# Optimization experiments

Hardware: AMD Instinct MI355X
Metric: run time of the kernel (lower is better)

The kernel has to match this reference:

```python
import jax, jax.numpy as jnp
from jax import lax
import numpy as np

Vw, Vc, TAGS = 50000, 200, 600
WE, CE, CC, H = 128, 48, 64, 256   # word emb, char emb, char cnn out, encoder hidden
B, T, CL, LMAX = 64, 96, 16, 24    # batch, seq, chars-per-word, lemma max len
HD = H // 2                        # per-direction LSTM hidden
BOS = 3


def _conv1d_same(x, w, b):
    # x: [N, Cin, L], w: [Cout, Cin, K] -> [N, Cout, L]
    y = lax.conv_general_dilated(x, w, (1,), 'SAME', dimension_numbers=('NCH', 'OIH', 'NCH'))
    return y + b[None, :, None]


def _lstm(x, wih, whh, b, reverse):
    # x: [B, T, D]; torch-gate-order LSTM (i, f, g, o); returns [B, T, HD]
    n = x.shape[0]
    def step(carry, xt):
        h, c = carry
        g = xt @ wih.T + h @ whh.T + b
        i, f, gg, o = jnp.split(g, 4, axis=-1)
        c = jax.nn.sigmoid(f) * c + jax.nn.sigmoid(i) * jnp.tanh(gg)
        h = jax.nn.sigmoid(o) * jnp.tanh(c)
        return (h, c), h
    init = (jnp.zeros((n, HD), x.dtype), jnp.zeros((n, HD), x.dtype))
    _, hs = lax.scan(step, init, jnp.swapaxes(x, 0, 1), reverse=reverse)
    return jnp.swapaxes(hs, 0, 1)


def setup_inputs() -> dict:
    key = jax.random.key(0)
    ks = jax.random.split(key, 26)
    g = lambda k, shape: jax.random.normal(k, shape, jnp.float32) * 0.05
    d = {}
    d['word_ids'] = jax.random.randint(ks[0], (B, T), 0, Vw)
    d['char_ids'] = jax.random.randint(ks[1], (B, T, CL), 0, Vc)
    d['word_emb'] = g(ks[2], (Vw, WE)).at[0].set(0.0)          # padding_idx=0
    d['char_emb'] = g(ks[3], (Vc, CE)).at[0].set(0.0)
    d['char_conv_w'] = g(ks[4], (CC, CE, 3))
    d['char_conv_b'] = g(ks[5], (CC,))
    DIN = WE + CC
    d['lstm_fw_wih'] = g(ks[6], (4 * HD, DIN)); d['lstm_fw_whh'] = g(ks[7], (4 * HD, HD)); d['lstm_fw_b'] = g(ks[8], (4 * HD,))
    d['lstm_bw_wih'] = g(ks[9], (4 * HD, DIN)); d['lstm_bw_whh'] = g(ks[10], (4 * HD, HD)); d['lstm_bw_b'] = g(ks[11], (4 * HD,))
    d['tag_w'] = g(ks[12], (TAGS, H)); d['tag_b'] = g(ks[13], (TAGS,))
    d['lemma_emb'] = g(ks[14], (Vc, CE)).at[0].set(0.0)
    d['lemma_init_w'] = g(ks[15], (H, H)); d['lemma_init_b'] = g(ks[16], (H,))
    d['gru_wih'] = g(ks[17], (3 * H, CE)); d['gru_whh'] = g(ks[18], (3 * H, H))
    d['gru_bih'] = g(ks[19], (3 * H,)); d['gru_bhh'] = g(ks[20], (3 * H,))
    d['lemma_proj_w'] = g(ks[21], (Vc, H)); d['lemma_proj_b'] = g(ks[22], (Vc,))
    return d


def reference(word_ids, char_ids, word_emb, char_emb, char_conv_w, char_conv_b,
              lstm_fw_wih, lstm_fw_whh, lstm_fw_b, lstm_bw_wih, lstm_bw_whh, lstm_bw_b,
              tag_w, tag_b, lemma_emb, lemma_init_w, lemma_init_b,
              gru_wih, gru_whh, gru_bih, gru_bhh, lemma_proj_w, lemma_proj_b):
    bsz, tseq = word_ids.shape
    n = bsz * tseq
    # word + char encodings
    wv = word_emb[word_ids]                                   # [B,T,WE]
    ce = char_emb[char_ids].reshape(n, CL, CE)                # [N,CL,CE]
    cv = jax.nn.relu(_conv1d_same(jnp.swapaxes(ce, 1, 2), char_conv_w, char_conv_b)).max(axis=-1)
    enc_in = jnp.concatenate([wv, cv.reshape(bsz, tseq, CC)], axis=-1)
    # BiLSTM encoder
    hf = _lstm(enc_in, lstm_fw_wih, lstm_fw_whh, lstm_fw_b, reverse=False)
    hb = _lstm(enc_in, lstm_bw_wih, lstm_bw_whh, lstm_bw_b, reverse=True)
    enc = jnp.concatenate([hf, hb], axis=-1)                  # [B,T,H]
    tag_logits = enc @ tag_w.T + tag_b
    ef = enc.reshape(n, H)
    h0 = jnp.tanh(ef @ lemma_init_w.T + lemma_init_b)
    prev0 = jnp.full((n,), BOS, dtype=jnp.int32)
    def dec_step(carry, _):
        h, prev = carry
        e = lemma_emb[prev]                                   # [N,CE]
        gi = e @ gru_wih.T + gru_bih
        gh = h @ gru_whh.T + gru_bhh
        ir, iz, inn = jnp.split(gi, 3, axis=-1)
        hr, hz, hn = jnp.split(gh, 3, axis=-1)
        r = jax.nn.sigmoid(ir + hr)
        z = jax.nn.sigmoid(iz + hz)
        nn_ = jnp.tanh(inn + r * hn)
        h = (1.0 - z) * nn_ + z * h
        logits = h @ lemma_proj_w.T + lemma_proj_b            # [N,Vc]
        return (h, jnp.argmax(logits, axis=-1).astype(jnp.int32)), logits
    _, ls = lax.scan(dec_step, (h0, prev0), None, length=LMAX)  # [LMAX,N,Vc]
    lemma_logits = jnp.moveaxis(ls, 0, 1).reshape(bsz, tseq, LMAX, Vc)
    return tag_logits, lemma_logits
```

## Files before the change

kernel.cpp:

```cpp
#include <hip/hip_runtime.h>
#include <hip/hip_bf16.h>
#include <math.h>

typedef float f4 __attribute__((ext_vector_type(4)));
typedef __attribute__((ext_vector_type(8))) short short8;

#define NTAGS 600
#define CEw   48
#define HH    256
#define TSEQ  96
#define CLW   16
#define LMAXD 24
#define NROWS 6144
#define DIN   192
#define VCD   200

__device__ __forceinline__ float sigf(float x){ return 1.0f/(1.0f+expf(-x)); }
__device__ __forceinline__ ushort bhi_u(float v){ __hip_bfloat16 h = __float2bfloat16(v); return *(ushort*)&h; }
__device__ __forceinline__ float ub_f(ushort u){ __hip_bfloat16 h = *(__hip_bfloat16*)&u; return __bfloat162float(h); }

template<int ACT, int HS, int KK>
__global__ __launch_bounds__(256)
void gemm3_k(const ushort* __restrict__ Ahi, const ushort* __restrict__ Alo,
             const ushort* __restrict__ Bhi, const ushort* __restrict__ Blo,
             const float* __restrict__ bias, float* __restrict__ C,
             ushort* __restrict__ Hhi, ushort* __restrict__ Hlo,
             int Nc, int ldC)
{
    __shared__ __align__(16) ushort As[128 * 64];
    __shared__ __align__(16) ushort Bs[128 * 64];
    const int tid = threadIdx.x;
    const int m0 = blockIdx.x * 128;
    const int n0 = blockIdx.y * 128;
    const int w = tid >> 6, l = tid & 63;
    const int wr = (w >> 1) * 64, wc = (w & 1) * 64;
    f4 acc[4][4];
    #pragma unroll
    for (int i = 0; i < 4; ++i)
        #pragma unroll
        for (int j = 0; j < 4; ++j) acc[i][j] = (f4){0.f,0.f,0.f,0.f};

    #pragma unroll
    for (int seg = 0; seg < 3; ++seg) {
        const ushort* Ap = (seg == 1) ? Alo : Ahi;
        const ushort* Bp = (seg == 2) ? Blo : Bhi;
        #pragma unroll
        for (int kt = 0; kt < KK; kt += 64) {
            #pragma unroll
            for (int i = 0; i < 4; ++i) {
                int c = w * 4 + i;
                int row = c * 8 + (l >> 3);
                int col16 = l & 7;
                __builtin_amdgcn_global_load_lds(
                    (const __attribute__((address_space(1))) void*)(Ap + (size_t)(m0 + row) * KK + kt + col16 * 8),
                    (__attribute__((address_space(3))) void*)((char*)As + c * 1024 + l * 16), 16, 0, 0);
                __builtin_amdgcn_global_load_lds(
                    (const __attribute__((address_space(1))) void*)(Bp + (size_t)(n0 + row) * KK + kt + col16 * 8),
                    (__attribute__((address_space(3))) void*)((char*)Bs + c * 1024 + l * 16), 16, 0, 0);
            }
            __syncthreads();
            #pragma unroll
            for (int kk = 0; kk < 64; kk += 32) {
                short8 a[4], b[4];
                #pragma unroll
                for (int mf = 0; mf < 4; ++mf)
                    a[mf] = *(const short8*)(As + (wr + mf * 16 + (l & 15)) * 64 + kk + (l >> 4) * 8);
                #pragma unroll
                for (int nf = 0; nf < 4; ++nf)
                    b[nf] = *(const short8*)(Bs + (wc + nf * 16 + (l & 15)) * 64 + kk + (l >> 4) * 8);
                #pragma unroll
                for (int mf = 0; mf < 4; ++mf)
                    #pragma unroll
                    for (int nf = 0; nf < 4; ++nf)
                        acc[mf][nf] = __builtin_amdgcn_mfma_f32_16x16x32_bf16(a[mf], b[nf], acc[mf][nf], 0, 0, 0);
            }
            __syncthreads();
        }
    }
    #pragma unroll
    for (int nf = 0; nf < 4; ++nf) {
        int n = n0 + wc + nf * 16 + (l & 15);
        if (n >= Nc) continue;
        float bv = bias[n];
        #pragma unroll
        for (int mf = 0; mf < 4; ++mf) {
            int mrow = m0 + wr + mf * 16 + (l >> 4) * 4;
            #pragma unroll
            for (int q2 = 0; q2 < 4; ++q2) {
                float v = acc[mf][nf][q2] + bv;
                if (ACT == 1) v = tanhf(v);
                size_t o = (size_t)(mrow + q2) * ldC + n;
                C[o] = v;
                if (HS) {
                    ushort hi = bhi_u(v);
                    Hhi[o] = hi;
                    Hlo[o] = bhi_u(v - ub_f(hi));
                }
            }
        }
    }
}

__global__ __launch_bounds__(256)
void gemmC_k(const ushort* __restrict__ Ahi, const ushort* __restrict__ Alo,
             const ushort* __restrict__ Bhi, const ushort* __restrict__ Blo,
             const float* __restrict__ bias,
             float* __restrict__ gh, float* __restrict__ lem, int ncol_gh)
{
    __shared__ __align__(16) ushort AsH[128 * 64];
    __shared__ __align__(16) ushort AsL[128 * 64];
    __shared__ __align__(16) ushort BsH[128 * 64];
    __shared__ __align__(16) ushort BsL[128 * 64];
    const int tid = threadIdx.x;
    const int m0 = blockIdx.x * 128;
    const int n0 = blockIdx.y * 128;
    const int w = tid >> 6, l = tid & 63;
    const int wr = (w >> 1) * 64, wc = (w & 1) * 64;
    f4 acc[4][4];
    #pragma unroll
    for (int i = 0; i < 4; ++i)
        #pragma unroll
        for (int j = 0; j < 4; ++j) acc[i][j] = (f4){0.f,0.f,0.f,0.f};

    #pragma unroll
    for (int kt = 0; kt < 256; kt += 64) {
        #pragma unroll
        for (int i = 0; i < 4; ++i) {
            int c = w * 4 + i;
            int row = c * 8 + (l >> 3);
            int col16 = l & 7;
            size_t ga = (size_t)(m0 + row) * 256 + kt + col16 * 8;
            size_t gb = (size_t)(n0 + row) * 256 + kt + col16 * 8;
            int loff = c * 1024 + l * 16;
            __builtin_amdgcn_global_load_lds(
                (const __attribute__((address_space(1))) void*)(Ahi + ga),
                (__attribute__((address_space(3))) void*)((char*)AsH + loff), 16, 0, 0);
            __builtin_amdgcn_global_load_lds(
                (const __attribute__((address_space(1))) void*)(Alo + ga),
                (__attribute__((address_space(3))) void*)((char*)AsL + loff), 16, 0, 0);
            __builtin_amdgcn_global_load_lds(
                (const __attribute__((address_space(1))) void*)(Bhi + gb),
                (__attribute__((address_space(3))) void*)((char*)BsH + loff), 16, 0, 0);
            __builtin_amdgcn_global_load_lds(
                (const __attribute__((address_space(1))) void*)(Blo + gb),
                (__attribute__((address_space(3))) void*)((char*)BsL + loff), 16, 0, 0);
        }
        __syncthreads();
        #pragma unroll
        for (int kk = 0; kk < 64; kk += 32) {
            short8 ah[4], al[4], bh[4], bl[4];
            #pragma unroll
            for (int mf = 0; mf < 4; ++mf) {
                int off = (wr + mf * 16 + (l & 15)) * 64 + kk + (l >> 4) * 8;
                ah[mf] = *(const short8*)(AsH + off);
                al[mf] = *(const short8*)(AsL + off);
            }
            #pragma unroll
            for (int nf = 0; nf < 4; ++nf) {
                int off = (wc + nf * 16 + (l & 15)) * 64 + kk + (l >> 4) * 8;
                bh[nf] = *(const short8*)(BsH + off);
                bl[nf] = *(const short8*)(BsL + off);
            }
            #pragma unroll
            for (int mf = 0; mf < 4; ++mf)
                #pragma unroll
                for (int nf = 0; nf < 4; ++nf) {
                    acc[mf][nf] = __builtin_amdgcn_mfma_f32_16x16x32_bf16(ah[mf], bh[nf], acc[mf][nf], 0, 0, 0);
                    acc[mf][nf] = __builtin_amdgcn_mfma_f32_16x16x32_bf16(al[mf], bh[nf], acc[mf][nf], 0, 0, 0);
                    acc[mf][nf] = __builtin_amdgcn_mfma_f32_16x16x32_bf16(ah[mf], bl[nf], acc[mf][nf], 0, 0, 0);
                }
        }
        __syncthreads();
    }
    #pragma unroll
    for (int nf = 0; nf < 4; ++nf) {
        int col = n0 + wc + nf * 16 + (l & 15);
        float bv = bias[col];
        #pragma unroll
        for (int mf = 0; mf < 4; ++mf) {
            int mrow = m0 + wr + mf * 16 + (l >> 4) * 4;
            #pragma unroll
            for (int q2 = 0; q2 < 4; ++q2) {
                float v = acc[mf][nf][q2] + bv;
                int m = mrow + q2;
                if (col < ncol_gh) {
                    gh[(size_t)m * 768 + col] = v;
                } else {
                    int c2 = col - ncol_gh;
                    if (c2 < VCD && lem) lem[(size_t)m * (LMAXD * VCD) + c2] = v;
                }
            }
        }
    }
}

__global__ __launch_bounds__(256)
void argupd_k(const float* __restrict__ gh, const float* __restrict__ git,
              const float* __restrict__ lem, float* __restrict__ h,
              ushort* __restrict__ hhi, ushort* __restrict__ hlo)
{
    const int n = blockIdx.x, tid = threadIdx.x;
    __shared__ float sv[4];
    __shared__ int   si[4];
    __shared__ int   sprev;
    if (lem) {
        float v = (tid < VCD) ? lem[(size_t)n * (LMAXD * VCD) + tid] : -3.4e38f;
        int bi = tid;
        #pragma unroll
        for (int d = 1; d < 64; d <<= 1) {
            float ov = __shfl_xor(v, d);
            int   oi = __shfl_xor(bi, d);
            if (ov > v || (ov == v && oi < bi)) { v = ov; bi = oi; }
        }
        if ((tid & 63) == 0) { sv[tid >> 6] = v; si[tid >> 6] = bi; }
        __syncthreads();
        if (tid == 0) {
            float b = sv[0]; int bi2 = si[0];
            #pragma unroll
            for (int t2 = 1; t2 < 4; ++t2)
                if (sv[t2] > b || (sv[t2] == b && si[t2] < bi2)) { b = sv[t2]; bi2 = si[t2]; }
            sprev = bi2;
        }
    } else if (tid == 0) sprev = 3;
    __syncthreads();
    const int prev = sprev;
    const int j = tid;
    const float* g  = gh + (size_t)n * 768;
    const float* gi = git + (size_t)prev * 768;
    float r  = sigf(gi[j] + g[j]);
    float z  = sigf(gi[256 + j] + g[256 + j]);
    float nn = tanhf(gi[512 + j] + r * g[512 + j]);
    size_t o = (size_t)n * HH + j;
    float hv = (1.0f - z) * nn + z * h[o];
    h[o] = hv;
    ushort hi = bhi_u(hv);
    hhi[o] = hi;
    hlo[o] = bhi_u(hv - ub_f(hi));
}

__global__ __launch_bounds__(256)
void conv_k(const ushort* __restrict__ cehi, const ushort* __restrict__ celo,
            const ushort* __restrict__ wre, const float* __restrict__ conv_b,
            float* __restrict__ enc_in)
{
    __shared__ __align__(16) ushort Bs[2 * 64 * 192];
    const int tid = threadIdx.x;
    for (int i = tid; i < 2 * 64 * 192 / 8; i += 256)
        ((uint4*)Bs)[i] = ((const uint4*)wre)[i];
    __syncthreads();
    const int w = tid >> 6, l = tid & 63;
    const int p = l & 15, g = l >> 4;
    const int base = (blockIdx.x * 4 + w) * 8;
    for (int wi = 0; wi < 8; ++wi) {
        int n = base + wi;
        short8 ahi[6], alo[6];
        #pragma unroll
        for (int kt = 0; kt < 6; ++kt) {
            int t = kt >> 1;
            int e0 = (kt & 1) * 32 + g * 8;
            int rl = p + t - 1;
            bool val = (rl >= 0 && rl < 16);
            size_t off = (size_t)(n * 16 + rl) * 64 + e0;
            short8 z = (short8){0,0,0,0,0,0,0,0};
            ahi[kt] = val ? *(const short8*)(cehi + off) : z;
            alo[kt] = val ? *(const short8*)(celo + off) : z;
        }
        f4 acc[4];
        #pragma unroll
        for (int nf = 0; nf < 4; ++nf) acc[nf] = (f4){0.f,0.f,0.f,0.f};
        #pragma unroll
        for (int kt = 0; kt < 6; ++kt) {
            #pragma unroll
            for (int nf = 0; nf < 4; ++nf) {
                int boff = (nf * 16 + (l & 15)) * 192 + kt * 32 + g * 8;
                short8 bh = *(const short8*)(Bs + boff);
                short8 bl = *(const short8*)(Bs + 12288 + boff);
                acc[nf] = __builtin_amdgcn_mfma_f32_16x16x32_bf16(ahi[kt], bh, acc[nf], 0, 0, 0);
                acc[nf] = __builtin_amdgcn_mfma_f32_16x16x32_bf16(alo[kt], bh, acc[nf], 0, 0, 0);
                acc[nf] = __builtin_amdgcn_mfma_f32_16x16x32_bf16(ahi[kt], bl, acc[nf], 0, 0, 0);
            }
        }
        #pragma unroll
        for (int nf = 0; nf < 4; ++nf) {
            float m = fmaxf(fmaxf(acc[nf][0], acc[nf][1]), fmaxf(acc[nf][2], acc[nf][3]));
            m = fmaxf(m, __shfl_xor(m, 16));
            m = fmaxf(m, __shfl_xor(m, 32));
            if (l < 16) {
                int c = nf * 16 + l;
                enc_in[(size_t)n * DIN + 128 + c] = fmaxf(0.0f, m + conv_b[c]);
            }
        }
    }
}

__global__ void repack192_k(const float* __restrict__ w, __hip_bfloat16* __restrict__ wre)
{
    int idx = blockIdx.x * 256 + threadIdx.x;
    if (idx >= 64 * 192) return;
    int kk = idx % 192, c = idx / 192;
    int t = kk >> 6, e = kk & 63;
    float v = (e < 48) ? w[(c * 48 + e) * 3 + t] : 0.0f;
    __hip_bfloat16 hi = __float2bfloat16(v);
    wre[idx] = hi;
    wre[64 * 192 + idx] = __float2bfloat16(v - __bfloat162float(hi));
}

__global__ void ce64_k(const int* __restrict__ char_ids, const float* __restrict__ char_emb,
                       __hip_bfloat16* __restrict__ hi, __hip_bfloat16* __restrict__ lo)
{
    size_t idx = (size_t)blockIdx.x * 256 + threadIdx.x;
    if (idx >= (size_t)NROWS * CLW * 64) return;
    int e = idx & 63;
    size_t r = idx >> 6;
    float v = (e < 48) ? char_emb[(size_t)char_ids[r] * CEw + e] : 0.0f;
    __hip_bfloat16 h = __float2bfloat16(v);
    hi[idx] = h;
    lo[idx] = __float2bfloat16(v - __bfloat162float(h));
}

__global__ void wv_k(const int* __restrict__ wid, const float* __restrict__ wemb,
                     float* __restrict__ enc_in)
{
    size_t idx = (size_t)blockIdx.x * 256 + threadIdx.x;
    if (idx >= (size_t)NROWS * 128) return;
    int e = idx & 127; size_t n = idx >> 7;
    enc_in[n * DIN + e] = wemb[(size_t)wid[n] * 128 + e];
}

__global__ void eisplit_k(const float* __restrict__ x, __hip_bfloat16* __restrict__ hi,
                          __hip_bfloat16* __restrict__ lo)
{
    size_t idx = (size_t)blockIdx.x * 256 + threadIdx.x;
    if (idx >= (size_t)NROWS * DIN) return;
    float v = x[idx];
    __hip_bfloat16 h = __float2bfloat16(v);
    hi[idx] = h;
    lo[idx] = __float2bfloat16(v - __bfloat162float(h));
}

__global__ void wsplit_k(const float* __restrict__ W, __hip_bfloat16* __restrict__ out,
                         int rows, int rowsPad, int K)
{
    int idx = blockIdx.x * 256 + threadIdx.x;
    if (idx >= rowsPad * K) return;
    int r = idx / K, k = idx - r * K;
    float v = (r < rows) ? W[(size_t)r * K + k] : 0.0f;
    __hip_bfloat16 hi = __float2bfloat16(v);
    out[idx] = hi;
    out[rowsPad * K + idx] = __float2bfloat16(v - __bfloat162float(hi));
}

__global__ void cmbsplit_k(const float* __restrict__ whh, const float* __restrict__ proj,
                           const float* __restrict__ bhh, const float* __restrict__ pb,
                           __hip_bfloat16* __restrict__ out, float* __restrict__ cbias)
{
    int idx = blockIdx.x * 256 + threadIdx.x;
    if (idx >= 1024 * 256) return;
    int r = idx >> 8, k = idx & 255;
    float v = (r < 768) ? whh[(size_t)r * 256 + k] : ((r < 968) ? proj[(size_t)(r - 768) * 256 + k] : 0.0f);
    __hip_bfloat16 hi = __float2bfloat16(v);
    out[idx] = hi;
    out[1024 * 256 + idx] = __float2bfloat16(v - __bfloat162float(hi));
    if (idx < 1024)
        cbias[idx] = (idx < 768) ? bhh[idx] : ((idx < 968) ? pb[idx - 768] : 0.0f);
}

__global__ void whht_k(const float* __restrict__ fw, const float* __restrict__ bw,
                       float* __restrict__ out)
{
    int idx = blockIdx.x * 256 + threadIdx.x;
    if (idx >= 131072) return;
    int q = idx & 3, j = (idx >> 2) & 127, k = (idx >> 9) & 127, d = idx >> 16;
    const float* w = d ? bw : fw;
    out[idx] = w[(size_t)(q * 128 + j) * 128 + k];
}

__global__ void gitab_k(const float* __restrict__ lemb, const float* __restrict__ wih,
                        const float* __restrict__ bih, float* __restrict__ git)
{
    int idx = blockIdx.x * 256 + threadIdx.x;
    if (idx >= VCD * 768) return;
    int g = idx % 768, v = idx / 768;
    float s = bih[g];
    #pragma unroll
    for (int k = 0; k < CEw; ++k) s = fmaf(lemb[v * CEw + k], wih[(size_t)g * CEw + k], s);
    git[idx] = s;
}

__global__ __launch_bounds__(1024, 4)
void lstm_k(const float* __restrict__ gi2, const float* __restrict__ whht,
            __hip_bfloat16* __restrict__ enc_hi, __hip_bfloat16* __restrict__ enc_lo)
{
    const int dir = blockIdx.x >> 6, b = blockIdx.x & 63;
    const int tid = threadIdx.x;
    const int j = tid & 127, q = tid >> 7;
    const float* gi = gi2 + (size_t)dir * NROWS * 512;
    const f4* wt = (const f4*)(whht + (size_t)dir * 65536);
    f4 wreg[16];
    #pragma unroll
    for (int kk = 0; kk < 16; ++kk) wreg[kk] = wt[(q * 16 + kk) * 128 + j];
    __shared__ float hbuf[128];
    __shared__ f4 part[8][128];
    float c = 0.0f;
    if (tid < 128) hbuf[tid] = 0.0f;
    float nai = 0.f, naf = 0.f, nag = 0.f, nao = 0.f;
    if (q == 0) {
        int t0 = dir ? (TSEQ - 1) : 0;
        const float* gr = gi + ((size_t)b * TSEQ + t0) * 512;
        nai = gr[j]; naf = gr[128 + j]; nag = gr[256 + j]; nao = gr[384 + j];
    }
    __syncthreads();
    for (int s = 0; s < TSEQ; ++s) {
        int t = dir ? (TSEQ - 1 - s) : s;
        size_t n = (size_t)b * TSEQ + t;
        float ai = nai, af = naf, ag = nag, ao = nao;
        const f4* hb = (const f4*)(hbuf + q * 16);
        f4 hh[4] = {hb[0], hb[1], hb[2], hb[3]};
        f4 p = (f4){0.f,0.f,0.f,0.f};
        #pragma unroll
        for (int kk = 0; kk < 16; ++kk) {
            float hv = hh[kk >> 2][kk & 3];
            p.x = fmaf(wreg[kk].x, hv, p.x);
            p.y = fmaf(wreg[kk].y, hv, p.y);
            p.z = fmaf(wreg[kk].z, hv, p.z);
            p.w = fmaf(wreg[kk].w, hv, p.w);
        }
        part[q][j] = p;
        __syncthreads();
        if (q == 0) {
            f4 sum = part[0][j];
            #pragma unroll
            for (int qq = 1; qq < 8; ++qq) {
                f4 pp = part[qq][j];
                sum.x += pp.x; sum.y += pp.y; sum.z += pp.z; sum.w += pp.w;
            }
            ai += sum.x; af += sum.y; ag += sum.z; ao += sum.w;
            c = sigf(af) * c + sigf(ai) * tanhf(ag);
            float h = sigf(ao) * tanhf(c);
            hbuf[j] = h;
            size_t o = n * HH + dir * 128 + j;
            __hip_bfloat16 hi = __float2bfloat16(h);
            enc_hi[o] = hi;
            enc_lo[o] = __float2bfloat16(h - __bfloat162float(hi));
            if (s + 1 < TSEQ) {
                int t2 = dir ? (TSEQ - 2 - s) : (s + 1);
                const float* gr2 = gi + ((size_t)b * TSEQ + t2) * 512;
                nai = gr2[j]; naf = gr2[128 + j]; nag = gr2[256 + j]; nao = gr2[384 + j];
            }
        }
        __syncthreads();
    }
}

extern "C" void kernel_launch(void* const* d_in, const int* in_sizes, int n_in,
                              void* d_out, int out_size, void* d_ws, size_t ws_size,
                              hipStream_t stream)
{
    const int*   word_ids = (const int*)d_in[0];
    const int*   char_ids = (const int*)d_in[1];
    const float* word_emb = (const float*)d_in[2];
    const float* char_emb = (const float*)d_in[3];
    const float* conv_w   = (const float*)d_in[4];
    const float* conv_b   = (const float*)d_in[5];
    const float* fw_wih   = (const float*)d_in[6];
    const float* fw_whh   = (const float*)d_in[7];
    const float* fw_b     = (const float*)d_in[8];
    const float* bw_wih   = (const float*)d_in[9];
    const float* bw_whh   = (const float*)d_in[10];
    const float* bw_b     = (const float*)d_in[11];
    const float* tag_w    = (const float*)d_in[12];
    const float* tag_b    = (const float*)d_in[13];
    const float* lemma_emb= (const float*)d_in[14];
    const float* init_w   = (const float*)d_in[15];
    const float* init_b   = (const float*)d_in[16];
    const float* gru_wih  = (const float*)d_in[17];
    const float* gru_whh  = (const float*)d_in[18];
    const float* gru_bih  = (const float*)d_in[19];
    const float* gru_bhh  = (const float*)d_in[20];
    const float* proj_w   = (const float*)d_in[21];
    const float* proj_b   = (const float*)d_in[22];

    char* ws = (char*)d_ws;
    float* enc_in = (float*)(ws);
    __hip_bfloat16* ei_hi = (__hip_bfloat16*)(ws + 4718592);
    __hip_bfloat16* ei_lo = (__hip_bfloat16*)(ws + 7077888);
    __hip_bfloat16* enc_hi = (__hip_bfloat16*)(ws);
    __hip_bfloat16* enc_lo = (__hip_bfloat16*)(ws + 3145728);
    char* R1 = ws + 9437184;
    __hip_bfloat16* ce_hi = (__hip_bfloat16*)R1;
    __hip_bfloat16* ce_lo = (__hip_bfloat16*)(R1 + 12582912);
    float* gi2 = (float*)R1;
    float* gh  = (float*)R1;
    __hip_bfloat16* cmb_ext = (__hip_bfloat16*)(R1 + 18874368);
    float* cmb_bias = (float*)(R1 + 18874368 + 1048576);
    float* hdec = (float*)(ws + 34603008);
    __hip_bfloat16* h_hi = (__hip_bfloat16*)(ws + 40894464);
    __hip_bfloat16* h_lo = (__hip_bfloat16*)(ws + 44040192);
    float* git  = (float*)(ws + 47185920);
    float* whht = (float*)(ws + 47800320);
    __hip_bfloat16* wre_ext  = (__hip_bfloat16*)(ws + 48349184);
    __hip_bfloat16* wfw_ext  = (__hip_bfloat16*)(ws + 48398336);
    __hip_bfloat16* wbw_ext  = (__hip_bfloat16*)(ws + 48791552);
    __hip_bfloat16* tag_ext  = (__hip_bfloat16*)(ws + 49184768);
    __hip_bfloat16* init_ext = (__hip_bfloat16*)(ws + 49840128);

    float* out_tag = (float*)d_out;
    float* out_lem = out_tag + (size_t)NROWS * NTAGS;

    repack192_k<<<48, 256, 0, stream>>>(conv_w, wre_ext);
    ce64_k<<<24576, 256, 0, stream>>>(char_ids, char_emb, ce_hi, ce_lo);
    wv_k<<<3072, 256, 0, stream>>>(word_ids, word_emb, enc_in);
    conv_k<<<192, 256, 0, stream>>>((const ushort*)ce_hi, (const ushort*)ce_lo,
                                    (const ushort*)wre_ext, conv_b, enc_in);
    eisplit_k<<<4608, 256, 0, stream>>>(enc_in, ei_hi, ei_lo);
    wsplit_k<<<384, 256, 0, stream>>>(fw_wih, wfw_ext, 512, 512, 192);
    wsplit_k<<<384, 256, 0, stream>>>(bw_wih, wbw_ext, 512, 512, 192);

    gemm3_k<0,0,192><<<dim3(48,4), 256, 0, stream>>>((const ushort*)ei_hi, (const ushort*)ei_lo,
        (const ushort*)wfw_ext, (const ushort*)(wfw_ext + 512*192), fw_b, gi2,
        nullptr, nullptr, 512, 512);
    gemm3_k<0,0,192><<<dim3(48,4), 256, 0, stream>>>((const ushort*)ei_hi, (const ushort*)ei_lo,
        (const ushort*)wbw_ext, (const ushort*)(wbw_ext + 512*192), bw_b, gi2 + (size_t)NROWS*512,
        nullptr, nullptr, 512, 512);
    whht_k<<<512, 256, 0, stream>>>(fw_whh, bw_whh, whht);
    lstm_k<<<128, 1024, 0, stream>>>(gi2, whht, enc_hi, enc_lo);

    cmbsplit_k<<<1024, 256, 0, stream>>>(gru_whh, proj_w, gru_bhh, proj_b, cmb_ext, cmb_bias);
    wsplit_k<<<640, 256, 0, stream>>>(tag_w, tag_ext, 600, 640, 256);
    wsplit_k<<<256, 256, 0, stream>>>(init_w, init_ext, 256, 256, 256);
    gitab_k<<<600, 256, 0, stream>>>(lemma_emb, gru_wih, gru_bih, git);
    gemm3_k<0,0,256><<<dim3(48,5), 256, 0, stream>>>((const ushort*)enc_hi, (const ushort*)enc_lo,
        (const ushort*)tag_ext, (const ushort*)(tag_ext + 640*256), tag_b, out_tag,
        nullptr, nullptr, NTAGS, NTAGS);
    gemm3_k<1,1,256><<<dim3(48,2), 256, 0, stream>>>((const ushort*)enc_hi, (const ushort*)enc_lo,
        (const ushort*)init_ext, (const ushort*)(init_ext + 256*256), init_b, hdec,
        (ushort*)h_hi, (ushort*)h_lo, 256, 256);

    const ushort* cmb_hi = (const ushort*)cmb_ext;
    const ushort* cmb_lo = cmb_hi + 1024 * 256;
    for (int s = 0; s < LMAXD; ++s) {
        float* lem = (s > 0) ? (out_lem + (size_t)(s - 1) * VCD) : nullptr;
        gemmC_k<<<dim3(48,8), 256, 0, stream>>>((const ushort*)h_hi, (const ushort*)h_lo,
            cmb_hi, cmb_lo, cmb_bias, gh, lem, 768);
        argupd_k<<<NROWS, 256, 0, stream>>>(gh, git, lem, hdec, (ushort*)h_hi, (ushort*)h_lo);
    }
    gemmC_k<<<dim3(48,2), 256, 0, stream>>>((const ushort*)h_hi, (const ushort*)h_lo,
        cmb_hi + 768 * 256, cmb_lo + 768 * 256, cmb_bias + 768,
        nullptr, out_lem + (size_t)(LMAXD - 1) * VCD, 0);
}
```

Before: 1.043 ms.

## Stream decoder GEMM operands from global memory with smaller M tiles; drop fp32 hidden state

The per-step decoder GEMM no longer stages A/B tiles through LDS with global_load_lds and barriers. It uses 64-row M tiles (twice the blocks) and loads MFMA operand fragments straight from global memory through the cache. The argmax/GRU update kernel now rebuilds the previous hidden state from the bf16 hi/lo split instead of a separate fp32 array, which removes one read and one write per element. It also remaps block indices so rows are grouped across tiles. The costs are redundant global loads of B across waves, and a hidden state limited to roughly 16-bit mantissa precision over 24 steps.

```diff
diff --git a/kernel.cpp b/kernel.cpp
--- a/kernel.cpp
+++ b/kernel.cpp
@@ -107,77 +107,46 @@
              const float* __restrict__ bias,
              float* __restrict__ gh, float* __restrict__ lem, int ncol_gh)
 {
-    __shared__ __align__(16) ushort AsH[128 * 64];
-    __shared__ __align__(16) ushort AsL[128 * 64];
-    __shared__ __align__(16) ushort BsH[128 * 64];
-    __shared__ __align__(16) ushort BsL[128 * 64];
     const int tid = threadIdx.x;
-    const int m0 = blockIdx.x * 128;
+    const int m0 = blockIdx.x * 64;
     const int n0 = blockIdx.y * 128;
     const int w = tid >> 6, l = tid & 63;
-    const int wr = (w >> 1) * 64, wc = (w & 1) * 64;
-    f4 acc[4][4];
-    #pragma unroll
-    for (int i = 0; i < 4; ++i)
+    const int wr = (w >> 1) * 32, wc = (w & 1) * 64;
+    const int lr = l & 15, lc = (l >> 4) * 8;
+    f4 acc[2][4];
+    #pragma unroll
+    for (int i = 0; i < 2; ++i)
         #pragma unroll
         for (int j = 0; j < 4; ++j) acc[i][j] = (f4){0.f,0.f,0.f,0.f};
 
-    #pragma unroll
-    for (int kt = 0; kt < 256; kt += 64) {
-        #pragma unroll
-        for (int i = 0; i < 4; ++i) {
-            int c = w * 4 + i;
-            int row = c * 8 + (l >> 3);
-            int col16 = l & 7;
-            size_t ga = (size_t)(m0 + row) * 256 + kt + col16 * 8;
-            size_t gb = (size_t)(n0 + row) * 256 + kt + col16 * 8;
-            int loff = c * 1024 + l * 16;
-            __builtin_amdgcn_global_load_lds(
-                (const __attribute__((address_space(1))) void*)(Ahi + ga),
-                (__attribute__((address_space(3))) void*)((char*)AsH + loff), 16, 0, 0);
-            __builtin_amdgcn_global_load_lds(
-                (const __attribute__((address_space(1))) void*)(Alo + ga),
-                (__attribute__((address_space(3))) void*)((char*)AsL + loff), 16, 0, 0);
-            __builtin_amdgcn_global_load_lds(
-                (const __attribute__((address_space(1))) void*)(Bhi + gb),
-                (__attribute__((address_space(3))) void*)((char*)BsH + loff), 16, 0, 0);
-            __builtin_amdgcn_global_load_lds(
-                (const __attribute__((address_space(1))) void*)(Blo + gb),
-                (__attribute__((address_space(3))) void*)((char*)BsL + loff), 16, 0, 0);
-        }
-        __syncthreads();
-        #pragma unroll
-        for (int kk = 0; kk < 64; kk += 32) {
-            short8 ah[4], al[4], bh[4], bl[4];
-            #pragma unroll
-            for (int mf = 0; mf < 4; ++mf) {
-                int off = (wr + mf * 16 + (l & 15)) * 64 + kk + (l >> 4) * 8;
-                ah[mf] = *(const short8*)(AsH + off);
-                al[mf] = *(const short8*)(AsL + off);
-            }
-            #pragma unroll
-            for (int nf = 0; nf < 4; ++nf) {
-                int off = (wc + nf * 16 + (l & 15)) * 64 + kk + (l >> 4) * 8;
-                bh[nf] = *(const short8*)(BsH + off);
-                bl[nf] = *(const short8*)(BsL + off);
-            }
-            #pragma unroll
-            for (int mf = 0; mf < 4; ++mf)
-                #pragma unroll
-                for (int nf = 0; nf < 4; ++nf) {
-                    acc[mf][nf] = __builtin_amdgcn_mfma_f32_16x16x32_bf16(ah[mf], bh[nf], acc[mf][nf], 0, 0, 0);
-                    acc[mf][nf] = __builtin_amdgcn_mfma_f32_16x16x32_bf16(al[mf], bh[nf], acc[mf][nf], 0, 0, 0);
-                    acc[mf][nf] = __builtin_amdgcn_mfma_f32_16x16x32_bf16(ah[mf], bl[nf], acc[mf][nf], 0, 0, 0);
-                }
-        }
-        __syncthreads();
+    const size_t arow0 = (size_t)(m0 + wr + lr) * 256;
+    const size_t arow1 = arow0 + 16 * 256;
+    #pragma unroll 4
+    for (int kt = 0; kt < 256; kt += 32) {
+        const int col = kt + lc;
+        short8 ah0 = *(const short8*)(Ahi + arow0 + col);
+        short8 ah1 = *(const short8*)(Ahi + arow1 + col);
+        short8 al0 = *(const short8*)(Alo + arow0 + col);
+        short8 al1 = *(const short8*)(Alo + arow1 + col);
+        #pragma unroll
+        for (int nf = 0; nf < 4; ++nf) {
+            size_t brow = (size_t)(n0 + wc + nf * 16 + lr) * 256 + col;
+            short8 bh = *(const short8*)(Bhi + brow);
+            short8 bl = *(const short8*)(Blo + brow);
+            acc[0][nf] = __builtin_amdgcn_mfma_f32_16x16x32_bf16(ah0, bh, acc[0][nf], 0, 0, 0);
+            acc[0][nf] = __builtin_amdgcn_mfma_f32_16x16x32_bf16(al0, bh, acc[0][nf], 0, 0, 0);
+            acc[0][nf] = __builtin_amdgcn_mfma_f32_16x16x32_bf16(ah0, bl, acc[0][nf], 0, 0, 0);
+            acc[1][nf] = __builtin_amdgcn_mfma_f32_16x16x32_bf16(ah1, bh, acc[1][nf], 0, 0, 0);
+            acc[1][nf] = __builtin_amdgcn_mfma_f32_16x16x32_bf16(al1, bh, acc[1][nf], 0, 0, 0);
+            acc[1][nf] = __builtin_amdgcn_mfma_f32_16x16x32_bf16(ah1, bl, acc[1][nf], 0, 0, 0);
+        }
     }
     #pragma unroll
     for (int nf = 0; nf < 4; ++nf) {
         int col = n0 + wc + nf * 16 + (l & 15);
         float bv = bias[col];
         #pragma unroll
-        for (int mf = 0; mf < 4; ++mf) {
+        for (int mf = 0; mf < 2; ++mf) {
             int mrow = m0 + wr + mf * 16 + (l >> 4) * 4;
             #pragma unroll
             for (int q2 = 0; q2 < 4; ++q2) {
@@ -187,7 +156,8 @@
                     gh[(size_t)m * 768 + col] = v;
                 } else {
                     int c2 = col - ncol_gh;
-                    if (c2 < VCD && lem) lem[(size_t)m * (LMAXD * VCD) + c2] = v;
+                    if (c2 < VCD && lem)
+                        lem[(size_t)m * (LMAXD * VCD) + c2] = v;
                 }
             }
         }
@@ -196,10 +166,14 @@
 
 __global__ __launch_bounds__(256)
 void argupd_k(const float* __restrict__ gh, const float* __restrict__ git,
-              const float* __restrict__ lem, float* __restrict__ h,
+              const float* __restrict__ lem,
               ushort* __restrict__ hhi, ushort* __restrict__ hlo)
 {
-    const int n = blockIdx.x, tid = threadIdx.x;
+    const int bid = blockIdx.x;
+    const int x = bid & 7, r = bid >> 3;
+    const int i = r >> 6, jrow = r & 63;
+    const int n = ((x + (i << 3)) << 6) + jrow;
+    const int tid = threadIdx.x;
     __shared__ float sv[4];
     __shared__ int   si[4];
     __shared__ int   sprev;
@@ -227,12 +201,12 @@
     const int j = tid;
     const float* g  = gh + (size_t)n * 768;
     const float* gi = git + (size_t)prev * 768;
-    float r  = sigf(gi[j] + g[j]);
+    float rg = sigf(gi[j] + g[j]);
     float z  = sigf(gi[256 + j] + g[256 + j]);
-    float nn = tanhf(gi[512 + j] + r * g[512 + j]);
+    float nn = tanhf(gi[512 + j] + rg * g[512 + j]);
     size_t o = (size_t)n * HH + j;
-    float hv = (1.0f - z) * nn + z * h[o];
-    h[o] = hv;
+    float hold = ub_f(hhi[o]) + ub_f(hlo[o]);
+    float hv = (1.0f - z) * nn + z * hold;
     ushort hi = bhi_u(hv);
     hhi[o] = hi;
     hlo[o] = bhi_u(hv - ub_f(hi));
@@ -540,11 +514,11 @@
     const ushort* cmb_lo = cmb_hi + 1024 * 256;
     for (int s = 0; s < LMAXD; ++s) {
         float* lem = (s > 0) ? (out_lem + (size_t)(s - 1) * VCD) : nullptr;
-        gemmC_k<<<dim3(48,8), 256, 0, stream>>>((const ushort*)h_hi, (const ushort*)h_lo,
+        gemmC_k<<<dim3(96,8), 256, 0, stream>>>((const ushort*)h_hi, (const ushort*)h_lo,
             cmb_hi, cmb_lo, cmb_bias, gh, lem, 768);
-        argupd_k<<<NROWS, 256, 0, stream>>>(gh, git, lem, hdec, (ushort*)h_hi, (ushort*)h_lo);
-    }
-    gemmC_k<<<dim3(48,2), 256, 0, stream>>>((const ushort*)h_hi, (const ushort*)h_lo,
+        argupd_k<<<NROWS, 256, 0, stream>>>(gh, git, lem, (ushort*)h_hi, (ushort*)h_lo);
+    }
+    gemmC_k<<<dim3(96,2), 256, 0, stream>>>((const ushort*)h_hi, (const ushort*)h_lo,
         cmb_hi + 768 * 256, cmb_lo + 768 * 256, cmb_bias + 768,
         nullptr, out_lem + (size_t)(LMAXD - 1) * VCD, 0);
 }
```

Result: slower. 1.445 ms (+38.5%).
